# Optimization experiments

Measured on AMD Instinct MI355X. Metric: run time of the kernel, lower is better.

Reference implementation:

```python
import jax, jax.numpy as jnp
import numpy as np

MD = 4  # max displacement -> (2*MD+1)**2 = 81 output channels

def setup_inputs() -> dict:
    key = jax.random.key(0)
    k1, k2 = jax.random.split(key)
    B, C, H, W = 4, 128, 128, 256
    t1 = jax.random.normal(k1, (B, C, H, W), dtype=jnp.float32)
    t2 = jax.random.normal(k2, (B, C, H, W), dtype=jnp.float32)
    return {"t1": t1, "t2": t2}

def reference(t1, t2):
    # PWC-Net correlation: for each displacement (dy,dx) in [-MD,MD]^2,
    # corr[b, d, y, x] = mean_c t1[b,c,y,x] * t2[b,c,y+dy,x+dx]
    B, C, H, W = t1.shape
    t2p = jnp.pad(t2, ((0, 0), (0, 0), (MD, MD), (MD, MD)))
    outs = []
    for dy in range(2 * MD + 1):
        for dx in range(2 * MD + 1):
            shifted = t2p[:, :, dy:dy + H, dx:dx + W]  # (B,C,H,W)
            outs.append(jnp.mean(t1 * shifted, axis=1))  # (B,H,W)
    return jnp.stack(outs, axis=1)  # (B, 81, H, W)
```

## Files before the change

### kernel.cpp

```cpp
#include <hip/hip_runtime.h>

#define MD   4
#define B_   4
#define C_   128
#define H_   128
#define W_   256
#define ND   9

typedef float  float4v __attribute__((ext_vector_type(4)));
typedef float  f32x4   __attribute__((ext_vector_type(4)));
typedef short  bf16x8  __attribute__((ext_vector_type(8)));
typedef unsigned int u32;
typedef u32    u32x4   __attribute__((ext_vector_type(4)));

#define TS ((size_t)B_ * H_ * 4 * W_ * 32)

static __device__ __forceinline__ unsigned short f2bf(float f) {
    u32 u = __float_as_uint(f);
    u32 r = (u + 0x7fffu + ((u >> 16) & 1u)) >> 16;
    return (unsigned short)r;
}

__global__ __launch_bounds__(256, 2)
void convert_one(const float* __restrict__ src0,
                 unsigned short* __restrict__ dst0) {
    const int bid = blockIdx.x;
    const int kc  = bid & 3;
    const int y   = (bid >> 2) & (H_ - 1);
    const int b   = bid >> 9;
    const int x   = threadIdx.x;
    const float* src = src0 + ((size_t)(b * C_ + kc * 32) * H_ + y) * W_ + x;
    const size_t hw = (size_t)H_ * W_;

    float f[32];
    #pragma unroll
    for (int k = 0; k < 32; ++k) f[k] = src[(size_t)k * hw];

    unsigned short* dst =
        dst0 + ((((size_t)(b * H_ + y)) * 4 + kc) * W_ + x) * 32;
    #pragma unroll
    for (int q = 0; q < 4; ++q) {
        u32x4 pk;
        #pragma unroll
        for (int j = 0; j < 4; ++j)
            pk[j] = (u32)f2bf(f[q * 8 + 2 * j]) |
                    ((u32)f2bf(f[q * 8 + 2 * j + 1]) << 16);
        *(u32x4*)(dst + q * 8) = pk;
    }
}

__global__ __launch_bounds__(512, 2)
void corr_mfma5(const unsigned short* __restrict__ ws,
                float* __restrict__ out) {
    __shared__ float scr[8][2 * 16 * 33];

    const int tid = threadIdx.x;
    const int l   = tid & 63;
    const int w   = tid >> 6;
    const int bid = blockIdx.x;
    const int xcd = bid & 7;
    const int xh  = xcd >> 2;
    const int ypq = xcd & 3;
    const int rst = bid >> 3;
    const int b   = rst >> 4;
    const int yp  = ypq * 16 + (rst & 15);
    const int y0  = yp * 2;
    const int ln  = l & 15;
    const int kg  = l >> 4;
    const int X0  = (xh * 8 + w) * 16;
    const float scale = 1.0f / (float)C_;
    const bf16x8 z8 = (bf16x8)(short)0;
    const unsigned short* t1w = ws;
    const unsigned short* t2w = ws + TS;

    f32x4 aA0[ND], aA1[ND], aB0[ND], aB1[ND];
    #pragma unroll
    for (int r = 0; r < ND; ++r) {
        aA0[r] = (f32x4)0.0f; aA1[r] = (f32x4)0.0f;
        aB0[r] = (f32x4)0.0f; aB1[r] = (f32x4)0.0f;
    }

    int col0 = X0 - 8 + ln;
    int col1 = X0 + 8 + ln;
    const bool ob0 = col0 < 0;
    const bool ob1 = col1 > W_ - 1;
    col0 = ob0 ? 0 : col0;
    col1 = ob1 ? W_ - 1 : col1;

    #pragma unroll
    for (int kc = 0; kc < 4; ++kc) {
        const unsigned short* a_base =
            t1w + ((((size_t)(b * H_ + y0)) * 4 + kc) * W_) * 32;
        const bf16x8 fA = *(const bf16x8*)(a_base + (size_t)(X0 + ln) * 32 + kg * 8);
        const bf16x8 fB = *(const bf16x8*)(a_base + (size_t)4 * W_ * 32
                                                  + (size_t)(X0 + ln) * 32 + kg * 8);

        #pragma unroll
        for (int r = 0; r < ND + 1; ++r) {
            const int row = y0 + r - MD;
            if (0 <= row && row < H_) {
                const unsigned short* b_base =
                    t2w + ((((size_t)(b * H_ + row)) * 4 + kc) * W_) * 32;
                bf16x8 b0 = *(const bf16x8*)(b_base + (size_t)col0 * 32 + kg * 8);
                bf16x8 b1 = *(const bf16x8*)(b_base + (size_t)col1 * 32 + kg * 8);
                b0 = ob0 ? z8 : b0;
                b1 = ob1 ? z8 : b1;
                if (r < ND) {
                    aA0[r] = __builtin_amdgcn_mfma_f32_16x16x32_bf16(fA, b0, aA0[r], 0, 0, 0);
                    aA1[r] = __builtin_amdgcn_mfma_f32_16x16x32_bf16(fA, b1, aA1[r], 0, 0, 0);
                }
                if (r >= 1) {
                    aB0[r-1] = __builtin_amdgcn_mfma_f32_16x16x32_bf16(fB, b0, aB0[r-1], 0, 0, 0);
                    aB1[r-1] = __builtin_amdgcn_mfma_f32_16x16x32_bf16(fB, b1, aB1[r-1], 0, 0, 0);
                }
            }
        }
    }

    float* sw = scr[w];

    #pragma unroll
    for (int r = 0; r < ND; ++r) {
        const int row = y0 + r - MD;
        const bool liv = (0 <= row && row < H_);
        #pragma unroll
        for (int i = 0; i < 4; ++i) {
            sw[(kg * 4 + i) * 33 + ln]       = aA0[r][i];
            sw[528 + (kg * 4 + i) * 33 + ln] = aA1[r][i];
        }
        #pragma unroll
        for (int i = 0; i < 3; ++i) {
            const int dx = i * 4 + kg;
            if (dx < ND) {
                const int m  = ln;
                const int md = m + dx;
                const int idx = (md < 12) ? (m * 33 + md + 4)
                                          : (528 + m * 33 + md - 12);
                const float v = liv ? sw[idx] * scale : 0.0f;
                out[((((size_t)b * 81) + r * ND + dx) * H_ + y0) * W_ + X0 + m] = v;
            }
        }
    }
    #pragma unroll
    for (int r = 0; r < ND; ++r) {
        const int row = y0 + 1 + r - MD;
        const bool liv = (0 <= row && row < H_);
        #pragma unroll
        for (int i = 0; i < 4; ++i) {
            sw[(kg * 4 + i) * 33 + ln]       = aB0[r][i];
            sw[528 + (kg * 4 + i) * 33 + ln] = aB1[r][i];
        }
        #pragma unroll
        for (int i = 0; i < 3; ++i) {
            const int dx = i * 4 + kg;
            if (dx < ND) {
                const int m  = ln;
                const int md = m + dx;
                const int idx = (md < 12) ? (m * 33 + md + 4)
                                          : (528 + m * 33 + md - 12);
                const float v = liv ? sw[idx] * scale : 0.0f;
                out[((((size_t)b * 81) + r * ND + dx) * H_ + (y0 + 1)) * W_ + X0 + m] = v;
            }
        }
    }
}

__global__ __launch_bounds__(9 * 64, 3)
void corr_fallback(const float* __restrict__ t1,
                   const float* __restrict__ t2,
                   float* __restrict__ out) {
    const int tid  = threadIdx.x;
    const int lane = tid & 63;
    const int w    = tid >> 6;
    const int bid  = blockIdx.x;
    const int swz  = (bid & 7) * 32 + (bid >> 3);
    const int yp   = swz & 63;
    const int b    = swz >> 6;
    const int y0   = yp * 2;
    const int half = lane >> 5;
    const int lx   = lane & 31;
    const int x0   = lx * 8;
    const int yrow = y0 + half;
    const int yy   = yrow + w - MD;
    const bool live = (0 <= yy) && (yy < H_);
    const int  yc  = yy < 0 ? 0 : (yy > H_ - 1 ? H_ - 1 : yy);
    const float sc = live ? (1.0f / (float)C_) : 0.0f;
    const bool lm  = (lx == 0);
    const bool rm  = (lx == 31);
    const int offL = lm ? 0 : -4;
    const int offR = rm ? 0 :  8;

    float acc[ND][8];
    #pragma unroll
    for (int dx = 0; dx < ND; ++dx)
        #pragma unroll
        for (int j = 0; j < 8; ++j) acc[dx][j] = 0.0f;

    const float* p1 = t1 + (((size_t)(b * C_)) * H_ + yrow) * W_ + x0;
    const float* p2 = t2 + (((size_t)(b * C_)) * H_ + yc  ) * W_ + x0;
    const size_t chstr = (size_t)H_ * W_;

    #pragma unroll 2
    for (int c = 0; c < C_; ++c) {
        const float* pc1 = p1 + (size_t)c * chstr;
        const float* pc2 = p2 + (size_t)c * chstr;
        const float4v a0 = *(const float4v*)(pc1);
        const float4v a1 = *(const float4v*)(pc1 + 4);
        float4v wl = *(const float4v*)(pc2 + offL);
        const float4v v0 = *(const float4v*)(pc2);
        const float4v v1 = *(const float4v*)(pc2 + 4);
        float4v wr = *(const float4v*)(pc2 + offR);
        #pragma unroll
        for (int q = 0; q < 4; ++q) {
            wl[q] = lm ? 0.0f : wl[q];
            wr[q] = rm ? 0.0f : wr[q];
        }
        float win[16];
        #pragma unroll
        for (int q = 0; q < 4; ++q) {
            win[q] = wl[q]; win[4 + q] = v0[q];
            win[8 + q] = v1[q]; win[12 + q] = wr[q];
        }
        #pragma unroll
        for (int dx = 0; dx < ND; ++dx)
            #pragma unroll
            for (int j = 0; j < 8; ++j) {
                const float aj = (j < 4) ? a0[j] : a1[j - 4];
                acc[dx][j] = fmaf(aj, win[dx + j], acc[dx][j]);
            }
    }

    #pragma unroll
    for (int dx = 0; dx < ND; ++dx) {
        float4v o0, o1;
        #pragma unroll
        for (int j = 0; j < 4; ++j) {
            o0[j] = acc[dx][j] * sc;
            o1[j] = acc[dx][4 + j] * sc;
        }
        const size_t oidx =
            (((size_t)(b * ND * ND) + w * ND + dx) * H_ + yrow) * W_ + x0;
        *(float4v*)&out[oidx]     = o0;
        *(float4v*)&out[oidx + 4] = o1;
    }
}

extern "C" void kernel_launch(void* const* d_in, const int* in_sizes, int n_in,
                              void* d_out, int out_size, void* d_ws, size_t ws_size,
                              hipStream_t stream) {
    const float* t1 = (const float*)d_in[0];
    const float* t2 = (const float*)d_in[1];
    float* out      = (float*)d_out;
    const size_t need = 2 * TS * sizeof(unsigned short);
    if (ws_size >= need) {
        unsigned short* ws = (unsigned short*)d_ws;
        convert_one<<<dim3(B_ * H_ * 4), 256, 0, stream>>>(t1, ws);
        convert_one<<<dim3(B_ * H_ * 4), 256, 0, stream>>>(t2, ws + TS);
        corr_mfma5<<<dim3(B_ * H_), 512, 0, stream>>>(ws, out);
    } else {
        corr_fallback<<<dim3(B_ * H_ / 2), 9 * 64, 0, stream>>>(t1, t2, out);
    }
}
```

Measured before the change: 80.04 us.

## Fuse t1 bf16 conversion into correlation kernel via double-buffered LDS staging

Removes the separate conversion launch for t1. The correlation kernel now reads t1 fp32 directly from global memory, converts it to bf16 in registers and stages it in a double-buffered shared-memory tile per channel chunk, with the next chunk's load overlapped with the current chunk's MFMAs. This saves one kernel launch plus a full write and re-read of the t1 workspace, at the cost of extra LDS use, block-wide barriers and in-kernel conversion work. The workspace requirement is halved.

```diff
diff --git a/kernel.cpp b/kernel.cpp
--- a/kernel.cpp
+++ b/kernel.cpp
@@ -50,9 +50,11 @@
 }
 
 __global__ __launch_bounds__(512, 2)
-void corr_mfma5(const unsigned short* __restrict__ ws,
+void corr_mfma7(const float* __restrict__ t1,
+                const unsigned short* __restrict__ t2w,
                 float* __restrict__ out) {
     __shared__ float scr[8][2 * 16 * 33];
+    __shared__ __align__(16) unsigned short aS[2][2][128][32];
 
     const int tid = threadIdx.x;
     const int l   = tid & 63;
@@ -70,8 +72,10 @@
     const int X0  = (xh * 8 + w) * 16;
     const float scale = 1.0f / (float)C_;
     const bf16x8 z8 = (bf16x8)(short)0;
-    const unsigned short* t1w = ws;
-    const unsigned short* t2w = ws + TS;
+    const size_t hw = (size_t)H_ * W_;
+
+    const int q  = tid >> 7;
+    const int xl = tid & 127;
 
     f32x4 aA0[ND], aA1[ND], aB0[ND], aB1[ND];
     #pragma unroll
@@ -87,13 +91,40 @@
     col0 = ob0 ? 0 : col0;
     col1 = ob1 ? W_ - 1 : col1;
 
+    float f[16];
+#define ALOAD(kc_)                                                          \
+    {                                                                       \
+        _Pragma("unroll")                                                   \
+        for (int i = 0; i < 16; ++i) {                                      \
+            const int cl = (i >> 1) + 8 * q;                                \
+            const int yy_ = i & 1;                                          \
+            f[i] = t1[((size_t)(b * C_ + (kc_) * 32 + cl) * H_              \
+                       + y0 + yy_) * W_ + xh * 128 + xl];                   \
+        }                                                                   \
+    }
+#define AWRITE(buf_)                                                        \
+    {                                                                       \
+        bf16x8 w0, w1;                                                      \
+        _Pragma("unroll")                                                   \
+        for (int j = 0; j < 8; ++j) {                                       \
+            w0[j] = (short)f2bf(f[2 * j]);                                  \
+            w1[j] = (short)f2bf(f[2 * j + 1]);                              \
+        }                                                                   \
+        *(bf16x8*)&aS[buf_][0][xl][q * 8] = w0;                             \
+        *(bf16x8*)&aS[buf_][1][xl][q * 8] = w1;                             \
+    }
+
+    ALOAD(0);
+    AWRITE(0);
+    __syncthreads();
+
     #pragma unroll
     for (int kc = 0; kc < 4; ++kc) {
-        const unsigned short* a_base =
-            t1w + ((((size_t)(b * H_ + y0)) * 4 + kc) * W_) * 32;
-        const bf16x8 fA = *(const bf16x8*)(a_base + (size_t)(X0 + ln) * 32 + kg * 8);
-        const bf16x8 fB = *(const bf16x8*)(a_base + (size_t)4 * W_ * 32
-                                                  + (size_t)(X0 + ln) * 32 + kg * 8);
+        const int buf = kc & 1;
+        if (kc < 3) ALOAD(kc + 1);
+
+        const bf16x8 fA = *(const bf16x8*)&aS[buf][0][w * 16 + ln][kg * 8];
+        const bf16x8 fB = *(const bf16x8*)&aS[buf][1][w * 16 + ln][kg * 8];
 
         #pragma unroll
         for (int r = 0; r < ND + 1; ++r) {
@@ -115,7 +146,12 @@
                 }
             }
         }
-    }
+
+        if (kc < 3) AWRITE(buf ^ 1);
+        __syncthreads();
+    }
+#undef ALOAD
+#undef AWRITE
 
     float* sw = scr[w];
 
@@ -211,15 +247,15 @@
         const float4v v1 = *(const float4v*)(pc2 + 4);
         float4v wr = *(const float4v*)(pc2 + offR);
         #pragma unroll
-        for (int q = 0; q < 4; ++q) {
-            wl[q] = lm ? 0.0f : wl[q];
-            wr[q] = rm ? 0.0f : wr[q];
+        for (int qq = 0; qq < 4; ++qq) {
+            wl[qq] = lm ? 0.0f : wl[qq];
+            wr[qq] = rm ? 0.0f : wr[qq];
         }
         float win[16];
         #pragma unroll
-        for (int q = 0; q < 4; ++q) {
-            win[q] = wl[q]; win[4 + q] = v0[q];
-            win[8 + q] = v1[q]; win[12 + q] = wr[q];
+        for (int qq = 0; qq < 4; ++qq) {
+            win[qq] = wl[qq]; win[4 + qq] = v0[qq];
+            win[8 + qq] = v1[qq]; win[12 + qq] = wr[qq];
         }
         #pragma unroll
         for (int dx = 0; dx < ND; ++dx)
@@ -251,12 +287,11 @@
     const float* t1 = (const float*)d_in[0];
     const float* t2 = (const float*)d_in[1];
     float* out      = (float*)d_out;
-    const size_t need = 2 * TS * sizeof(unsigned short);
+    const size_t need = TS * sizeof(unsigned short);
     if (ws_size >= need) {
         unsigned short* ws = (unsigned short*)d_ws;
-        convert_one<<<dim3(B_ * H_ * 4), 256, 0, stream>>>(t1, ws);
-        convert_one<<<dim3(B_ * H_ * 4), 256, 0, stream>>>(t2, ws + TS);
-        corr_mfma5<<<dim3(B_ * H_), 512, 0, stream>>>(ws, out);
+        convert_one<<<dim3(B_ * H_ * 4), 256, 0, stream>>>(t2, ws);
+        corr_mfma7 <<<dim3(B_ * H_), 512, 0, stream>>>(t1, ws, out);
     } else {
         corr_fallback<<<dim3(B_ * H_ / 2), 9 * 64, 0, stream>>>(t1, t2, out);
     }
```

After: 69.03 us. 1.16x faster.
